# Kernel tuning notes

Hardware: AMD Instinct MI355X
Metric: run time of the kernel (lower is better)

The kernel has to match this reference:

```python
import jax, jax.numpy as jnp
import numpy as np

B, S, P, D, H, R = 2, 2048, 1024, 2048, 16, 16
DH = D // H  # 128


def _rope(t, cos, sin):
    # t: [B,S,H,DH]; cos/sin: [S, DH//2]; complex pair rotation
    t2 = t.reshape(t.shape[0], t.shape[1], t.shape[2], DH // 2, 2)
    a, b = t2[..., 0], t2[..., 1]
    c = cos[None, :, None, :]
    s = sin[None, :, None, :]
    out = jnp.stack([a * c - b * s, a * s + b * c], axis=-1)
    return out.reshape(t.shape)


def setup_inputs() -> dict:
    key = jax.random.key(0)
    ks = jax.random.split(key, 16)
    sc = 1.0 / np.sqrt(D)
    inv_freq = 1.0 / (10000.0 ** (np.arange(0, DH, 2, dtype=np.float32) / DH))
    pos = (P + np.arange(S, dtype=np.float32))[:, None] * inv_freq[None, :]
    i_idx = np.arange(S)[:, None]
    j_idx = np.arange(P + S)[None, :]
    mask = np.where(j_idx <= P + i_idx, 0.0, -1e9).astype(np.float32)
    return {
        "x": jax.random.normal(ks[0], (B, S, D), jnp.float32),
        "freqs_cos": jnp.asarray(np.cos(pos)),
        "freqs_sin": jnp.asarray(np.sin(pos)),
        "mask": jnp.asarray(mask)[None, None],
        "prev_key": jax.random.normal(ks[1], (B, P, H, DH), jnp.float32),
        "prev_value": jax.random.normal(ks[2], (B, P, H, DH), jnp.float32),
        "pooled_scale": jax.random.uniform(ks[3], (B, 1), jnp.float32),
        "wq": jax.random.normal(ks[4], (D, D), jnp.float32) * sc,
        "wk": jax.random.normal(ks[5], (D, D), jnp.float32) * sc,
        "wv": jax.random.normal(ks[6], (D, D), jnp.float32) * sc,
        "wo": jax.random.normal(ks[7], (D, D), jnp.float32) * sc,
        "wq_A": jax.random.normal(ks[8], (D, R), jnp.float32) * sc,
        "wq_B": jax.random.normal(ks[9], (R, D), jnp.float32) * 0.02,
        "wk_A": jax.random.normal(ks[10], (D, R), jnp.float32) * sc,
        "wk_B": jax.random.normal(ks[11], (R, D), jnp.float32) * 0.02,
        "wv_A": jax.random.normal(ks[12], (D, R), jnp.float32) * sc,
        "wv_B": jax.random.normal(ks[13], (R, D), jnp.float32) * 0.02,
        "wo_A": jax.random.normal(ks[14], (D, R), jnp.float32) * sc,
        "wo_B": jax.random.normal(ks[15], (R, D), jnp.float32) * 0.02,
    }


def reference(x, freqs_cos, freqs_sin, mask, prev_key, prev_value, pooled_scale,
              wq, wk, wv, wo, wq_A, wq_B, wk_A, wk_B, wv_A, wv_B, wo_A, wo_B):
    ps = pooled_scale[:, None, :]  # [B,1,1] per-batch LoRA scale
    xq = x @ wq.T + (x @ wq_A) @ wq_B * ps
    xk = x @ wk.T + (x @ wk_A) @ wk_B * ps
    xv = x @ wv.T + (x @ wv_A) @ wv_B * ps
    xq = xq.reshape(B, S, H, DH)
    xk = xk.reshape(B, S, H, DH)
    xv = xv.reshape(B, S, H, DH)
    xq = _rope(xq, freqs_cos, freqs_sin)
    xk = _rope(xk, freqs_cos, freqs_sin)
    keys = jnp.concatenate([prev_key, xk], axis=1)      # [B,P+S,H,DH]
    values = jnp.concatenate([prev_value, xv], axis=1)
    q = xq.transpose(0, 2, 1, 3)       # [B,H,S,DH]
    k = keys.transpose(0, 2, 1, 3)     # [B,H,P+S,DH]
    v = values.transpose(0, 2, 1, 3)
    scores = jnp.einsum("bhqd,bhkd->bhqk", q, k) / jnp.sqrt(jnp.float32(DH))
    scores = scores + mask
    probs = jax.nn.softmax(scores.astype(jnp.float32), axis=-1).astype(q.dtype)
    out = jnp.einsum("bhqk,bhkd->bhqd", probs, v)
    out = out.transpose(0, 2, 1, 3).reshape(B, S, D)
    return out @ wo.T + (out @ wo_A) @ wo_B * ps
```

## Files before the change

kernel.cpp:

```cpp
#include <hip/hip_runtime.h>
#include <stdint.h>

#define BB 2
#define SS 2048
#define PP 1024
#define DD 2048
#define HH 16
#define RR 16
#define DHH 128
#define TT (PP + SS)
#define BSR (BB * SS)

typedef __attribute__((ext_vector_type(8))) _Float16 half8;
typedef __attribute__((ext_vector_type(4))) float f32x4;

typedef __attribute__((address_space(3))) unsigned int lds_uint;
typedef const __attribute__((address_space(1))) unsigned int glb_uint;
__device__ __forceinline__ void async_copy16(const void* g, void* l) {
    __builtin_amdgcn_global_load_lds((glb_uint*)g, (lds_uint*)l, 16, 0, 0);
}

__global__ __launch_bounds__(256) void cvt_f16x5_kernel(
    const float* __restrict__ s0, const float* __restrict__ s1,
    const float* __restrict__ s2, const float* __restrict__ s3,
    const float* __restrict__ s4,
    _Float16* __restrict__ dx, _Float16* __restrict__ dqkv,
    _Float16* __restrict__ dwo)
{
    const int seg = blockIdx.y;
    const float* in;
    _Float16* out;
    int n4;
    if (seg == 0)      { in = s0; out = dx;  n4 = (BSR * DD) / 4; }
    else if (seg == 4) { in = s4; out = dwo; n4 = (DD * DD) / 4; }
    else {
        in  = (seg == 1) ? s1 : (seg == 2) ? s2 : s3;
        out = dqkv + (size_t)(seg - 1) * DD * DD;
        n4  = (DD * DD) / 4;
    }
    int idx = blockIdx.x * 256 + threadIdx.x;
    int stride = gridDim.x * 256;
    for (int c = idx; c < n4; c += stride) {
        float4 v = *(const float4*)(in + (size_t)c * 4);
        union { _Float16 h[4]; uint2 u; } o;
        o.h[0] = (_Float16)v.x; o.h[1] = (_Float16)v.y;
        o.h[2] = (_Float16)v.z; o.h[3] = (_Float16)v.w;
        *(uint2*)(out + (size_t)c * 4) = o.u;
    }
}

__global__ __launch_bounds__(256) void lora_t_kernel(
    const float* __restrict__ A,
    const float* __restrict__ w0, const float* __restrict__ w1,
    const float* __restrict__ w2,
    float* __restrict__ tout)
{
    const float* wA = (blockIdx.z == 0) ? w0 : (blockIdx.z == 1) ? w1 : w2;
    int i  = blockIdx.x * 16 + (threadIdx.x >> 4);
    int r  = threadIdx.x & 15;
    int k0 = blockIdx.y * 512;
    const float* arow = A  + (size_t)i  * DD + k0;
    const float* wcol = wA + (size_t)k0 * RR + r;
    float acc = 0.f;
#pragma unroll 4
    for (int k = 0; k < 512; ++k)
        acc += arow[k] * wcol[k * RR];
    atomicAdd(&tout[(size_t)blockIdx.z * (BSR * RR) + (size_t)i * RR + r], acc);
}

__global__ __launch_bounds__(256) void lora_t_f16_kernel(
    const _Float16* __restrict__ A, const float* __restrict__ wA,
    float* __restrict__ tout)
{
    int i  = blockIdx.x * 16 + (threadIdx.x >> 4);
    int r  = threadIdx.x & 15;
    int k0 = blockIdx.y * 512;
    const _Float16* arow = A + (size_t)i * DD + k0;
    const float* wcol = wA + (size_t)k0 * RR + r;
    float acc = 0.f;
#pragma unroll 4
    for (int k = 0; k < 512; ++k)
        acc += (float)arow[k] * wcol[k * RR];
    atomicAdd(&tout[(size_t)i * RR + r], acc);
}

__global__ __launch_bounds__(256, 3) void gemm_f16_kernel(
    const _Float16* __restrict__ Ah, const _Float16* __restrict__ Wh,
    float* __restrict__ o0, float* __restrict__ o1, float* __restrict__ o2)
{
    __shared__ __align__(16) _Float16 As[128 * 32];
    __shared__ __align__(16) _Float16 Bs[128 * 32];
    const int tid  = threadIdx.x;
    const int wv   = tid >> 6;
    const int lane = tid & 63;
    const int ln   = lane & 15;
    const int quad = lane >> 4;
    const int i0   = blockIdx.x * 128;
    const int j0f  = blockIdx.y * 128;
    const int mat  = j0f >> 11;
    const int jloc = j0f & 2047;
    float* out_f = (mat == 0) ? o0 : (mat == 1) ? o1 : o2;
    const int mb   = (wv >> 1) * 4;
    const int nb   = (wv & 1) * 4;
    const int srow = wv * 32 + (lane >> 2);
    const int scol = (lane & 3) * 8;

    f32x4 zero = {0.f, 0.f, 0.f, 0.f};
    f32x4 acc[4][4];
#pragma unroll
    for (int a = 0; a < 4; ++a)
#pragma unroll
        for (int c = 0; c < 4; ++c) acc[a][c] = zero;

    const _Float16* gA = Ah + (size_t)(i0 + srow) * DD + scol;
    const _Float16* gB = Wh + (size_t)(j0f + srow) * DD + scol;
    _Float16* lA0 = As + (wv * 32) * 32;
    _Float16* lA1 = As + (wv * 32 + 16) * 32;
    _Float16* lB0 = Bs + (wv * 32) * 32;
    _Float16* lB1 = Bs + (wv * 32 + 16) * 32;

    for (int k0 = 0; k0 < DD; k0 += 32) {
        async_copy16(gA + k0, lA0);
        async_copy16(gA + (size_t)16 * DD + k0, lA1);
        async_copy16(gB + k0, lB0);
        async_copy16(gB + (size_t)16 * DD + k0, lB1);
        __syncthreads();
        half8 b[4];
#pragma unroll
        for (int nt = 0; nt < 4; ++nt)
            b[nt] = *(const half8*)&Bs[((nb + nt) * 16 + ln) * 32 + quad * 8];
#pragma unroll
        for (int mt = 0; mt < 4; ++mt) {
            half8 a = *(const half8*)&As[((mb + mt) * 16 + ln) * 32 + quad * 8];
#pragma unroll
            for (int nt = 0; nt < 4; ++nt)
                acc[mt][nt] = __builtin_amdgcn_mfma_f32_16x16x32_f16(a, b[nt], acc[mt][nt], 0, 0, 0);
        }
        __syncthreads();
    }

#pragma unroll
    for (int mt = 0; mt < 4; ++mt)
#pragma unroll
        for (int nt = 0; nt < 4; ++nt)
#pragma unroll
            for (int reg = 0; reg < 4; ++reg) {
                int row = i0 + (mb + mt) * 16 + quad * 4 + reg;
                int col = jloc + (nb + nt) * 16 + ln;
                out_f[(size_t)row * DD + col] = acc[mt][nt][reg];
            }
}

__global__ __launch_bounds__(256) void lora_add_kernel(
    const float* __restrict__ t, const float* __restrict__ wB,
    const float* __restrict__ ps, float* __restrict__ out)
{
    const int n4 = BSR * (DD / 4);
    int idx = blockIdx.x * 256 + threadIdx.x;
    int stride = gridDim.x * 256;
    for (int c = idx; c < n4; c += stride) {
        int i  = c >> 9;
        int j4 = c & 511;
        float psb = ps[i >> 11];
        const float* trow = t + (size_t)i * RR;
        float* op = out + (size_t)i * DD + j4 * 4;
        f32x4 acc = *(const f32x4*)op;
#pragma unroll
        for (int r = 0; r < 16; ++r) {
            float tv = psb * trow[r];
            f32x4 w = *(const f32x4*)(wB + (size_t)r * DD + j4 * 4);
#pragma unroll
            for (int q = 0; q < 4; ++q)
                acc[q] += tv * w[q];
        }
        *(f32x4*)op = acc;
    }
}

__global__ __launch_bounds__(256) void prev_scatter_kernel(
    const float* __restrict__ pk, const float* __restrict__ pv,
    _Float16* __restrict__ kh, _Float16* __restrict__ vTh)
{
    __shared__ __align__(16) _Float16 vt[128][72];
    const int pt = blockIdx.x, h = blockIdx.y;
    const int b = pt >> 4, p0 = (pt & 15) * 64;
    const int tid = threadIdx.x;
    const size_t bh = (size_t)(b * HH + h);
#pragma unroll
    for (int p = 0; p < 8; ++p) {
        int c = tid + 256 * p;
        int pl = c >> 5, c4 = (c & 31) * 4;
        float4 v4 = *(const float4*)(pk + (((size_t)(b * PP + p0 + pl)) * HH + h) * DHH + c4);
        union { _Float16 h4[4]; uint2 u; } o;
        o.h4[0] = (_Float16)v4.x; o.h4[1] = (_Float16)v4.y;
        o.h4[2] = (_Float16)v4.z; o.h4[3] = (_Float16)v4.w;
        *(uint2*)(kh + (bh * TT + p0 + pl) * DHH + c4) = o.u;
    }
#pragma unroll
    for (int p = 0; p < 8; ++p) {
        int c = tid + 256 * p;
        int pl = c >> 5, c4 = (c & 31) * 4;
        float4 v4 = *(const float4*)(pv + (((size_t)(b * PP + p0 + pl)) * HH + h) * DHH + c4);
        vt[c4 + 0][pl] = (_Float16)v4.x;
        vt[c4 + 1][pl] = (_Float16)v4.y;
        vt[c4 + 2][pl] = (_Float16)v4.z;
        vt[c4 + 3][pl] = (_Float16)v4.w;
    }
    __syncthreads();
#pragma unroll
    for (int p = 0; p < 4; ++p) {
        int c = tid + 256 * p;
        int d = c >> 3, c8 = (c & 7) * 8;
        *(half8*)(vTh + (bh * DHH + d) * TT + p0 + c8) = *(const half8*)&vt[d][c8];
    }
}

__global__ __launch_bounds__(256) void rope_scatter_kernel(
    const float* __restrict__ xq, const float* __restrict__ xk,
    const float* __restrict__ xv,
    const float* __restrict__ t_all,
    const float* __restrict__ wqB, const float* __restrict__ wkB,
    const float* __restrict__ wvB,
    const float* __restrict__ ps,
    const float* __restrict__ fcos, const float* __restrict__ fsin,
    _Float16* __restrict__ qh, _Float16* __restrict__ kh,
    _Float16* __restrict__ vTh)
{
    __shared__ float tS[64][48];
    __shared__ float wBs[3][16][128];
    __shared__ __align__(16) _Float16 vt[128][72];
    const int st = blockIdx.x, h = blockIdx.y;
    const int i0 = st * 64;
    const int b  = i0 >> 11;
    const int s0 = i0 & 2047;
    const int tid = threadIdx.x;
    const size_t bh = (size_t)(b * HH + h);
    const float QSC = 0.12753102f;

#pragma unroll
    for (int p = 0; p < 12; ++p) {
        int idx = tid + 256 * p;
        int w = idx >> 10, rem = idx & 1023;
        int sl = rem >> 4, r = rem & 15;
        tS[sl][w * 16 + r] = t_all[(size_t)w * (BSR * RR) + (size_t)(i0 + sl) * RR + r];
    }
#pragma unroll
    for (int w = 0; w < 3; ++w) {
        const float* src = (w == 0) ? wqB : (w == 1) ? wkB : wvB;
#pragma unroll
        for (int p = 0; p < 8; ++p) {
            int idx = tid + 256 * p;
            int r = idx >> 7, dd = idx & 127;
            wBs[w][r][dd] = src[(size_t)r * DD + h * DHH + dd];
        }
    }
    __syncthreads();
    const float psb = ps[b];

#pragma unroll
    for (int w = 0; w < 2; ++w) {
        const float* src = (w == 0) ? xq : xk;
        for (int p = 0; p < 16; ++p) {
            int pp = tid + 256 * p;
            int sl = pp >> 6, dd = pp & 63;
            int d = dd * 2;
            int i = i0 + sl, s = s0 + sl;
            float2 pr = *(const float2*)(src + (size_t)i * DD + h * DHH + d);
            float a = pr.x, b2 = pr.y;
            float la = 0.f, lb = 0.f;
#pragma unroll
            for (int r = 0; r < 16; ++r) {
                float tv = tS[sl][w * 16 + r];
                la += tv * wBs[w][r][d];
                lb += tv * wBs[w][r][d + 1];
            }
            a  += psb * la;
            b2 += psb * lb;
            float c  = fcos[(size_t)s * 64 + dd];
            float sn = fsin[(size_t)s * 64 + dd];
            float na = a * c - b2 * sn;
            float nb = a * sn + b2 * c;
            union { _Float16 h2[2]; unsigned u; } o;
            if (w == 0) {
                o.h2[0] = (_Float16)(na * QSC); o.h2[1] = (_Float16)(nb * QSC);
                *(unsigned*)(qh + (bh * SS + s) * DHH + d) = o.u;
            } else {
                o.h2[0] = (_Float16)na; o.h2[1] = (_Float16)nb;
                *(unsigned*)(kh + (bh * TT + PP + s) * DHH + d) = o.u;
            }
        }
    }
    for (int p = 0; p < 16; ++p) {
        int pp = tid + 256 * p;
        int sl = pp >> 6, dd = pp & 63;
        int d = dd * 2;
        int i = i0 + sl;
        float2 pr = *(const float2*)(xv + (size_t)i * DD + h * DHH + d);
        float a = pr.x, b2 = pr.y;
        float la = 0.f, lb = 0.f;
#pragma unroll
        for (int r = 0; r < 16; ++r) {
            float tv = tS[sl][32 + r];
            la += tv * wBs[2][r][d];
            lb += tv * wBs[2][r][d + 1];
        }
        a  += psb * la;
        b2 += psb * lb;
        vt[d][sl]     = (_Float16)a;
        vt[d + 1][sl] = (_Float16)b2;
    }
    __syncthreads();
#pragma unroll
    for (int p = 0; p < 4; ++p) {
        int c = tid + 256 * p;
        int d = c >> 3, c8 = (c & 7) * 8;
        *(half8*)(vTh + (bh * DHH + d) * TT + PP + s0 + c8) = *(const half8*)&vt[d][c8];
    }
}

__global__ __launch_bounds__(256) void attn_kernel(
    const _Float16* __restrict__ qh, const _Float16* __restrict__ kh,
    const _Float16* __restrict__ vTh, _Float16* __restrict__ attn_h)
{
    __shared__ __align__(16) _Float16 k_lds[64][136];
    __shared__ __align__(16) _Float16 v_lds[128][72];
    __shared__ __align__(16) _Float16 p_lds[4][16][72];
    const int lin = blockIdx.x;
    const int bh_i = lin & 31;
    const int t5   = lin >> 5;
    const int qtp  = (lin < 512) ? t5 : 47 - t5;
    const int h = bh_i & 15, b = bh_i >> 4;
    const int qbase = qtp * 64;
    const int ntiles = 17 + qtp;
    const int tid = threadIdx.x, wv = tid >> 6, lane = tid & 63;
    const int ln = lane & 15, quad = lane >> 4;
    const size_t bh = (size_t)(b * HH + h);

    half8 qfrag[4];
    {
        const _Float16* qrow = qh + (bh * SS + qbase + wv * 16 + ln) * DHH;
#pragma unroll
        for (int ks = 0; ks < 4; ++ks)
            qfrag[ks] = *(const half8*)(qrow + ks * 32 + quad * 8);
    }
    f32x4 zero = {0.f, 0.f, 0.f, 0.f};
    f32x4 O[8];
#pragma unroll
    for (int i = 0; i < 8; ++i) O[i] = zero;
    float l_part[4];
#pragma unroll
    for (int r = 0; r < 4; ++r) l_part[r] = 0.f;

    int offKg[4], offKl[4], offVg[4], offVl[4];
#pragma unroll
    for (int p = 0; p < 4; ++p) {
        int c = tid + 256 * p;
        int key = c >> 4, ck = (c & 15) * 8;
        offKg[p] = key * DHH + ck;
        offKl[p] = key * 136 + ck;
        int d = c >> 3, cv = (c & 7) * 8;
        offVg[p] = d * TT + cv;
        offVl[p] = d * 72 + cv;
    }
    const _Float16* kbase = kh + bh * (size_t)TT * DHH;
    const _Float16* vbase = vTh + bh * (size_t)DHH * TT;

    half8 k0r[4], v0r[4], k1r[4], v1r[4];
#pragma unroll
    for (int p = 0; p < 4; ++p) {
        k0r[p] = *(const half8*)(kbase + offKg[p]);
        v0r[p] = *(const half8*)(vbase + offVg[p]);
    }

#define ATTN_BODY(KT, KC, VC, KN, VN)                                          \
  {                                                                            \
    const int kb = (KT) * 64;                                                  \
    _Pragma("unroll")                                                          \
    for (int p = 0; p < 4; ++p) {                                              \
        *(half8*)((_Float16*)k_lds + offKl[p]) = KC[p];                        \
        *(half8*)((_Float16*)v_lds + offVl[p]) = VC[p];                        \
    }                                                                          \
    __syncthreads();                                                           \
    if ((KT) + 1 < ntiles) {                                                   \
        const _Float16* kg = kbase + (size_t)(kb + 64) * DHH;                  \
        const _Float16* vg = vbase + (kb + 64);                                \
        _Pragma("unroll")                                                      \
        for (int p = 0; p < 4; ++p) {                                          \
            KN[p] = *(const half8*)(kg + offKg[p]);                            \
            VN[p] = *(const half8*)(vg + offVg[p]);                            \
        }                                                                      \
    }                                                                          \
    f32x4 sv[4];                                                               \
    __builtin_amdgcn_s_setprio(1);                                             \
    _Pragma("unroll")                                                          \
    for (int nt = 0; nt < 4; ++nt) {                                           \
        half8 kf[4];                                                           \
        _Pragma("unroll")                                                      \
        for (int ks = 0; ks < 4; ++ks)                                         \
            kf[ks] = *(const half8*)&k_lds[nt * 16 + ln][ks * 32 + quad * 8];  \
        f32x4 sacc = zero;                                                     \
        _Pragma("unroll")                                                      \
        for (int ks = 0; ks < 4; ++ks)                                         \
            sacc = __builtin_amdgcn_mfma_f32_16x16x32_f16(qfrag[ks], kf[ks], sacc, 0, 0, 0); \
        sv[nt] = sacc;                                                         \
    }                                                                          \
    __builtin_amdgcn_s_setprio(0);                                             \
    const bool tail = ((KT) == ntiles - 1);                                    \
    _Pragma("unroll")                                                          \
    for (int nt = 0; nt < 4; ++nt)                                             \
        _Pragma("unroll")                                                      \
        for (int reg = 0; reg < 4; ++reg) {                                    \
            float z = sv[nt][reg];                                             \
            if (tail) {                                                        \
                int jj = nt * 16 + ln;                                         \
                int rg = wv * 16 + quad * 4 + reg;                             \
                if (jj > rg) z = -1e30f;                                       \
            }                                                                  \
            float pz = exp2f(z - 12.f);                                        \
            l_part[reg] += pz;                                                 \
            {                                                                  \
                int row = quad * 4 + reg;                                      \
                int cs  = (nt * 2 + (ln >> 3)) ^ ((row >> 1) & 7);             \
                p_lds[wv][row][cs * 8 + (ln & 7)] = (_Float16)pz;              \
            }                                                                  \
        }                                                                      \
    __builtin_amdgcn_s_setprio(1);                                             \
    _Pragma("unroll")                                                          \
    for (int kf2 = 0; kf2 < 2; ++kf2) {                                        \
        int cA = ((kf2 * 4 + quad) ^ ((ln >> 1) & 7)) * 8;                     \
        half8 pa = *(const half8*)&p_lds[wv][ln][cA];                          \
        _Pragma("unroll")                                                      \
        for (int d8 = 0; d8 < 8; ++d8) {                                       \
            half8 vb = *(const half8*)&v_lds[d8 * 16 + ln][kf2 * 32 + quad * 8]; \
            O[d8] = __builtin_amdgcn_mfma_f32_16x16x32_f16(pa, vb, O[d8], 0, 0, 0); \
        }                                                                      \
    }                                                                          \
    __builtin_amdgcn_s_setprio(0);                                             \
    __syncthreads();                                                           \
  }

    if (ntiles & 1) {
        ATTN_BODY(0, k0r, v0r, k1r, v1r);
        for (int kt = 1; kt < ntiles; kt += 2) {
            ATTN_BODY(kt,     k1r, v1r, k0r, v0r);
            ATTN_BODY(kt + 1, k0r, v0r, k1r, v1r);
        }
    } else {
        for (int kt = 0; kt < ntiles; kt += 2) {
            ATTN_BODY(kt,     k0r, v0r, k1r, v1r);
            ATTN_BODY(kt + 1, k1r, v1r, k0r, v0r);
        }
    }
#undef ATTN_BODY

#pragma unroll
    for (int reg = 0; reg < 4; ++reg) {
        float l = l_part[reg];
#pragma unroll
        for (int off = 1; off < 16; off <<= 1)
            l += __shfl_xor(l, off);
        l_part[reg] = 1.f / l;
    }
#pragma unroll
    for (int d8 = 0; d8 < 8; ++d8)
#pragma unroll
        for (int reg = 0; reg < 4; ++reg) {
            int row = qbase + wv * 16 + quad * 4 + reg;
            int col = h * DHH + d8 * 16 + ln;
            attn_h[((size_t)b * SS + row) * DD + col] =
                (_Float16)(O[d8][reg] * l_part[reg]);
        }
}

extern "C" void kernel_launch(void* const* d_in, const int* in_sizes, int n_in,
                              void* d_out, int out_size, void* d_ws, size_t ws_size,
                              hipStream_t stream) {
    const float* x    = (const float*)d_in[0];
    const float* fcos = (const float*)d_in[1];
    const float* fsin = (const float*)d_in[2];
    const float* pk   = (const float*)d_in[4];
    const float* pv   = (const float*)d_in[5];
    const float* ps   = (const float*)d_in[6];
    const float* wq   = (const float*)d_in[7];
    const float* wk   = (const float*)d_in[8];
    const float* wvw  = (const float*)d_in[9];
    const float* wo   = (const float*)d_in[10];
    const float* wqA  = (const float*)d_in[11];
    const float* wqB  = (const float*)d_in[12];
    const float* wkA  = (const float*)d_in[13];
    const float* wkB  = (const float*)d_in[14];
    const float* wvA  = (const float*)d_in[15];
    const float* wvB  = (const float*)d_in[16];
    const float* woA  = (const float*)d_in[17];
    const float* woB  = (const float*)d_in[18];
    float* out = (float*)d_out;

    float* t_all = (float*)d_ws;
    float* t_o   = t_all + 3 * BSR * RR;
    float* xq    = t_all + 4 * BSR * RR;
    float* xk    = xq + (size_t)BSR * DD;
    float* xv    = xk + (size_t)BSR * DD;
    _Float16* xh    = (_Float16*)(xv + (size_t)BSR * DD);
    _Float16* wqkvh = xh + (size_t)BSR * DD;
    _Float16* woh   = wqkvh + (size_t)3 * DD * DD;
    _Float16* qh_   = woh + (size_t)DD * DD;
    _Float16* kh_   = qh_ + (size_t)BB * HH * SS * DHH;
    _Float16* vTh   = kh_ + (size_t)BB * HH * TT * DHH;
    _Float16* attn_h = vTh + (size_t)BB * HH * DHH * TT;
    (void)ws_size; (void)in_sizes; (void)n_in; (void)out_size;

    hipMemsetAsync(t_all, 0, (size_t)4 * BSR * RR * sizeof(float), stream);

    cvt_f16x5_kernel<<<dim3(512, 5), 256, 0, stream>>>(x, wq, wk, wvw, wo,
                                                       xh, wqkvh, woh);

    lora_t_kernel<<<dim3(256, 4, 3), 256, 0, stream>>>(x, wqA, wkA, wvA, t_all);

    gemm_f16_kernel<<<dim3(32, 48), 256, 0, stream>>>(xh, wqkvh, xq, xk, xv);

    prev_scatter_kernel<<<dim3(32, 16), 256, 0, stream>>>(pk, pv, kh_, vTh);

    rope_scatter_kernel<<<dim3(64, 16), 256, 0, stream>>>(xq, xk, xv, t_all,
                                                          wqB, wkB, wvB, ps,
                                                          fcos, fsin,
                                                          qh_, kh_, vTh);

    attn_kernel<<<1024, 256, 0, stream>>>(qh_, kh_, vTh, attn_h);

    lora_t_f16_kernel<<<dim3(256, 4), 256, 0, stream>>>(attn_h, woA, t_o);

    gemm_f16_kernel<<<dim3(32, 16), 256, 0, stream>>>(attn_h, woh, out, out, out);

    lora_add_kernel<<<2048, 256, 0, stream>>>(t_o, woB, ps, out);
}
```

Measured before the change: 752.8 us.

## Fuse LoRA-A projections on f16 input, swap GEMM grid order, change P swizzle

The three LoRA down-projections now run in one kernel that reads the f16 copy of x once and accumulates all three rank-16 outputs, replacing three separate passes over the fp32 input. The GEMM grid axes are swapped so consecutive blocks walk the output columns, which changes how blocks share A and B tiles in L2. The LDS XOR swizzle for the probability tile in attention is changed to a quad-based pattern to alter bank-conflict behaviour. Using the f16 x for LoRA slightly reduces precision of the low-rank term.

```diff
diff --git a/kernel.cpp b/kernel.cpp
--- a/kernel.cpp
+++ b/kernel.cpp
@@ -49,23 +49,30 @@
     }
 }
 
-__global__ __launch_bounds__(256) void lora_t_kernel(
-    const float* __restrict__ A,
+__global__ __launch_bounds__(256) void lora_t3_kernel(
+    const _Float16* __restrict__ Ah,
     const float* __restrict__ w0, const float* __restrict__ w1,
     const float* __restrict__ w2,
     float* __restrict__ tout)
 {
-    const float* wA = (blockIdx.z == 0) ? w0 : (blockIdx.z == 1) ? w1 : w2;
     int i  = blockIdx.x * 16 + (threadIdx.x >> 4);
     int r  = threadIdx.x & 15;
     int k0 = blockIdx.y * 512;
-    const float* arow = A  + (size_t)i  * DD + k0;
-    const float* wcol = wA + (size_t)k0 * RR + r;
-    float acc = 0.f;
+    const _Float16* arow = Ah + (size_t)i * DD + k0;
+    const float* c0 = w0 + (size_t)k0 * RR + r;
+    const float* c1 = w1 + (size_t)k0 * RR + r;
+    const float* c2 = w2 + (size_t)k0 * RR + r;
+    float a0 = 0.f, a1 = 0.f, a2 = 0.f;
 #pragma unroll 4
-    for (int k = 0; k < 512; ++k)
-        acc += arow[k] * wcol[k * RR];
-    atomicAdd(&tout[(size_t)blockIdx.z * (BSR * RR) + (size_t)i * RR + r], acc);
+    for (int k = 0; k < 512; ++k) {
+        float av = (float)arow[k];
+        a0 += av * c0[k * RR];
+        a1 += av * c1[k * RR];
+        a2 += av * c2[k * RR];
+    }
+    atomicAdd(&tout[(size_t)0 * (BSR * RR) + (size_t)i * RR + r], a0);
+    atomicAdd(&tout[(size_t)1 * (BSR * RR) + (size_t)i * RR + r], a1);
+    atomicAdd(&tout[(size_t)2 * (BSR * RR) + (size_t)i * RR + r], a2);
 }
 
 __global__ __launch_bounds__(256) void lora_t_f16_kernel(
@@ -95,8 +102,8 @@
     const int lane = tid & 63;
     const int ln   = lane & 15;
     const int quad = lane >> 4;
-    const int i0   = blockIdx.x * 128;
-    const int j0f  = blockIdx.y * 128;
+    const int i0   = blockIdx.y * 128;
+    const int j0f  = blockIdx.x * 128;
     const int mat  = j0f >> 11;
     const int jloc = j0f & 2047;
     float* out_f = (mat == 0) ? o0 : (mat == 1) ? o1 : o2;
@@ -420,14 +427,14 @@
             l_part[reg] += pz;                                                 \
             {                                                                  \
                 int row = quad * 4 + reg;                                      \
-                int cs  = (nt * 2 + (ln >> 3)) ^ ((row >> 1) & 7);             \
+                int cs  = (nt * 2 + (ln >> 3)) ^ quad;                         \
                 p_lds[wv][row][cs * 8 + (ln & 7)] = (_Float16)pz;              \
             }                                                                  \
         }                                                                      \
     __builtin_amdgcn_s_setprio(1);                                             \
     _Pragma("unroll")                                                          \
     for (int kf2 = 0; kf2 < 2; ++kf2) {                                        \
-        int cA = ((kf2 * 4 + quad) ^ ((ln >> 1) & 7)) * 8;                     \
+        int cA = ((kf2 * 4 + quad) ^ (ln >> 2)) * 8;                           \
         half8 pa = *(const half8*)&p_lds[wv][ln][cA];                          \
         _Pragma("unroll")                                                      \
         for (int d8 = 0; d8 < 8; ++d8) {                                       \
@@ -514,9 +521,9 @@
     cvt_f16x5_kernel<<<dim3(512, 5), 256, 0, stream>>>(x, wq, wk, wvw, wo,
                                                        xh, wqkvh, woh);
 
-    lora_t_kernel<<<dim3(256, 4, 3), 256, 0, stream>>>(x, wqA, wkA, wvA, t_all);
-
-    gemm_f16_kernel<<<dim3(32, 48), 256, 0, stream>>>(xh, wqkvh, xq, xk, xv);
+    lora_t3_kernel<<<dim3(256, 4), 256, 0, stream>>>(xh, wqA, wkA, wvA, t_all);
+
+    gemm_f16_kernel<<<dim3(48, 32), 256, 0, stream>>>(xh, wqkvh, xq, xk, xv);
 
     prev_scatter_kernel<<<dim3(32, 16), 256, 0, stream>>>(pk, pv, kh_, vTh);
 
@@ -529,7 +536,7 @@
 
     lora_t_f16_kernel<<<dim3(256, 4), 256, 0, stream>>>(attn_h, woA, t_o);
 
-    gemm_f16_kernel<<<dim3(32, 16), 256, 0, stream>>>(attn_h, woh, out, out, out);
+    gemm_f16_kernel<<<dim3(16, 32), 256, 0, stream>>>(attn_h, woh, out, out, out);
 
     lora_add_kernel<<<2048, 256, 0, stream>>>(t_o, woB, ps, out);
 }
```

Result: faster. 680.8 us (-9.6%).
